# Optimization experiments

Hardware: AMD Instinct MI355X
Metric: run time of the kernel (lower is better)

Reference implementation:

```python
import jax, jax.numpy as jnp
import numpy as np

B, S, HID = 2, 2048, 1024
H, HKV, D = 16, 8, 128
G = H // HKV
EPS = 1e-6
ROPE_BASE = 1e6


def _rms_norm(x, w):
    # per-last-dim RMSNorm in fp32, matching QwenRMSNorm
    x32 = x.astype(jnp.float32)
    var = jnp.mean(x32 * x32, axis=-1, keepdims=True)
    return w * (x32 * jax.lax.rsqrt(var + EPS)).astype(x.dtype)


def _rotate_half(x):
    half = x.shape[-1] // 2
    return jnp.concatenate([-x[..., half:], x[..., :half]], axis=-1)


def setup_inputs() -> dict:
    key = jax.random.key(0)
    ks = jax.random.split(key, 6)
    return {
        "hidden_states": jax.random.normal(ks[0], (B, S, HID), dtype=jnp.float32),
        "position_ids": jnp.arange(S, dtype=jnp.int32),
        "Wq": jax.random.normal(ks[1], (HID, H * D), dtype=jnp.float32) * 0.02,
        "Wk": jax.random.normal(ks[2], (HID, HKV * D), dtype=jnp.float32) * 0.02,
        "Wv": jax.random.normal(ks[3], (HID, HKV * D), dtype=jnp.float32) * 0.02,
        "Wo": jax.random.normal(ks[4], (H * D, HID), dtype=jnp.float32) * 0.02,
        "q_norm_w": jnp.ones((D,), dtype=jnp.float32),
        "k_norm_w": jnp.ones((D,), dtype=jnp.float32),
    }


def reference(hidden_states, position_ids, Wq, Wk, Wv, Wo, q_norm_w, k_norm_w):
    b, s, _ = hidden_states.shape
    # projections
    q = (hidden_states @ Wq).reshape(b, s, H, D)
    k = (hidden_states @ Wk).reshape(b, s, HKV, D)
    v = (hidden_states @ Wv).reshape(b, s, HKV, D)
    # QK RMSNorm (per head_dim), then [B, heads, S, D]
    q = _rms_norm(q, q_norm_w).transpose(0, 2, 1, 3)
    k = _rms_norm(k, k_norm_w).transpose(0, 2, 1, 3)
    v = v.transpose(0, 2, 1, 3)
    # RoPE
    inv_freq = 1.0 / (ROPE_BASE ** (jnp.arange(0, D, 2, dtype=jnp.float32) / D))
    freqs = position_ids.astype(jnp.float32)[:, None] * inv_freq[None, :]  # [S, D/2]
    emb = jnp.concatenate([freqs, freqs], axis=-1)  # [S, D]
    cos = jnp.cos(emb)[None, None, :, :].astype(q.dtype)
    sin = jnp.sin(emb)[None, None, :, :].astype(q.dtype)
    q = q * cos + _rotate_half(q) * sin
    k = k * cos + _rotate_half(k) * sin
    # GQA attention without materializing repeated K/V:
    # q heads h = kh*G + g  <->  repeat_interleave(G, dim=1) of kv heads
    qg = q.reshape(b, HKV, G, s, D)
    scale = 1.0 / jnp.sqrt(jnp.asarray(D, dtype=q.dtype))
    scores = jnp.einsum('bhgqd,bhkd->bhgqk', qg, k) * scale  # [B,HKV,G,S,S]
    causal = jnp.tril(jnp.ones((s, s), dtype=bool))
    scores = jnp.where(causal[None, None, None, :, :], scores, jnp.finfo(scores.dtype).min)
    probs = jax.nn.softmax(scores, axis=-1)
    attn = jnp.einsum('bhgqk,bhkd->bhgqd', probs, v)  # [B,HKV,G,S,D]
    attn = attn.reshape(b, H, s, D).transpose(0, 2, 1, 3).reshape(b, s, H * D)
    out = attn @ Wo
    return out, k, v
```

## Files before the change

### kernel.cpp

```cpp
#include <hip/hip_runtime.h>

#define B_ 2
#define S_ 2048
#define HID_ 1024
#define H_ 16
#define HKV_ 8
#define D_ 128

typedef unsigned short u16;
typedef __attribute__((ext_vector_type(8))) short short8;
typedef __attribute__((ext_vector_type(4))) float f32x4;
typedef __attribute__((ext_vector_type(16))) float f32x16;
typedef __attribute__((ext_vector_type(2))) unsigned short u16x2;
typedef __attribute__((ext_vector_type(4))) unsigned short u16x4;
typedef const __attribute__((address_space(1))) void gvoid;
typedef __attribute__((address_space(3))) void svoid;

__device__ __forceinline__ u16 f2b(float f) {
  union { float f; unsigned u; } v; v.f = f;
  unsigned r = v.u + 0x7FFFu + ((v.u >> 16) & 1u);
  return (u16)(r >> 16);
}
__device__ __forceinline__ float b2f(u16 x) {
  union { unsigned u; float f; } v; v.u = ((unsigned)x) << 16; return v.f;
}

__device__ __forceinline__ float exp2_fast(float x) {
  float r; asm("v_exp_f32 %0, %1" : "=v"(r) : "v"(x)); return r;
}
__device__ __forceinline__ unsigned cvtpk_bf16(float lo, float hi) {
  unsigned r; asm("v_cvt_pk_bf16_f32 %0, %1, %2" : "=v"(r) : "v"(lo), "v"(hi)); return r;
}
__device__ __forceinline__ void vm_drain() {
  asm volatile("s_waitcnt vmcnt(0)" ::: "memory");
  __builtin_amdgcn_sched_barrier(0);
}

__global__ __launch_bounds__(256) void conv_bf16_kernel(const float* __restrict__ X,
                                                        u16* __restrict__ Y, int n4) {
  int i = blockIdx.x * 256 + threadIdx.x;
  if (i < n4) {
    const float4 v = ((const float4*)X)[i];
    u16x4 o = { f2b(v.x), f2b(v.y), f2b(v.z), f2b(v.w) };
    ((u16x4*)Y)[i] = o;
  }
}

template <bool PERM>
__global__ __launch_bounds__(256) void transpose_bf16_kernel(const float* __restrict__ W,
                                                             u16* __restrict__ Wt,
                                                             int K, int N) {
  __shared__ float t[32][33];
  const int nb = N >> 5;
  const int bx = blockIdx.x % nb;
  const int by = blockIdx.x / nb;
  const int tx = threadIdx.x & 31, ty = threadIdx.x >> 5;
#pragma unroll
  for (int i = 0; i < 32; i += 8)
    t[ty + i][tx] = W[(size_t)(by * 32 + ty + i) * N + bx * 32 + tx];
  __syncthreads();
#pragma unroll
  for (int i = 0; i < 32; i += 8) {
    int n = bx * 32 + ty + i;
    int nn;
    if (PERM) {
      int head = n >> 7, d = n & 127;
      int p = (d & 15) | (((d >> 6) & 1) << 4) | (((d >> 4) & 1) << 5) | (((d >> 5) & 1) << 6);
      nn = head * 128 + p;
    } else {
      nn = n;
    }
    Wt[(size_t)nn * K + by * 32 + tx] = f2b(t[tx][ty + i]);
  }
}

__global__ __launch_bounds__(256) void rope_table_kernel(const int* __restrict__ pid,
                                                         float* __restrict__ ct,
                                                         float* __restrict__ st) {
  int i = blockIdx.x * 256 + threadIdx.x;
  if (i >= 64 * S_) return;
  int f = i >> 11, s = i & 2047;
  double inv = exp2(-(double)f * (19.931568569324174 / 64.0));
  double ang = (double)pid[s] * inv;
  ct[i] = (float)cos(ang);
  st[i] = (float)sin(ang);
}

template <int M, int N, int K, int BM>
__global__ __launch_bounds__(256) void gemm_bt(const u16* __restrict__ A,
                                               const u16* __restrict__ Bt,
                                               float* __restrict__ C) {
  __shared__ u16 As[BM * 32];
  __shared__ u16 Bs[128 * 32];
  const int tid = threadIdx.x;
  const int w = tid >> 6;
  const int l = tid & 63;
  const int l15 = l & 15, lg = l >> 4;
  const int nbx = N / 128;
  const int bx = blockIdx.x % nbx, by = blockIdx.x / nbx;
  const int row0 = by * BM, col0 = bx * 128;
  const int wr = w >> 1, wc = w & 1;
  constexpr int MR = BM / 32;

  f32x4 acc[MR][4];
#pragma unroll
  for (int m = 0; m < MR; ++m)
#pragma unroll
    for (int n = 0; n < 4; ++n) acc[m][n] = (f32x4){0.f, 0.f, 0.f, 0.f};

  for (int k0 = 0; k0 < K; k0 += 32) {
    __syncthreads();
#pragma unroll
    for (int i = 0; i < BM / 64; ++i) {
      int c = i * 256 + tid;
      int r = c >> 2, cc = c & 3;
      const u16* sa = A + (size_t)(row0 + r) * K + k0 + cc * 8;
      __builtin_amdgcn_global_load_lds((gvoid*)sa, (svoid*)(As + (i * 256 + w * 64) * 8), 16, 0, 0);
    }
#pragma unroll
    for (int i = 0; i < 2; ++i) {
      int c = i * 256 + tid;
      int r = c >> 2, cc = c & 3;
      const u16* sb = Bt + (size_t)(col0 + r) * K + k0 + cc * 8;
      __builtin_amdgcn_global_load_lds((gvoid*)sb, (svoid*)(Bs + (i * 256 + w * 64) * 8), 16, 0, 0);
    }
    vm_drain();
    __syncthreads();
    short8 af[MR], bf[4];
#pragma unroll
    for (int m = 0; m < MR; ++m)
      af[m] = *(const short8*)(As + (wr * (BM / 2) + m * 16 + l15) * 32 + lg * 8);
#pragma unroll
    for (int n = 0; n < 4; ++n)
      bf[n] = *(const short8*)(Bs + (wc * 64 + n * 16 + l15) * 32 + lg * 8);
#pragma unroll
    for (int m = 0; m < MR; ++m)
#pragma unroll
      for (int n = 0; n < 4; ++n)
        acc[m][n] = __builtin_amdgcn_mfma_f32_16x16x32_bf16(af[m], bf[n], acc[m][n], 0, 0, 0);
  }
#pragma unroll
  for (int m = 0; m < MR; ++m)
#pragma unroll
    for (int n = 0; n < 4; ++n) {
      float* cp = C + (size_t)(row0 + wr * (BM / 2) + m * 16 + lg * 4) * N + col0 + wc * 64 + n * 16 + l15;
#pragma unroll
      for (int r = 0; r < 4; ++r) cp[(size_t)r * N] = acc[m][n][r];
    }
}

__global__ __launch_bounds__(256) void gemm_qkv_fused(const u16* __restrict__ A,
                                                      const u16* __restrict__ Bt,
                                                      const float* __restrict__ qnw,
                                                      const float* __restrict__ knw,
                                                      const float* __restrict__ ct_t,
                                                      const float* __restrict__ st_t,
                                                      u16* __restrict__ Qbb,
                                                      u16* __restrict__ Kbb,
                                                      float* __restrict__ kout,
                                                      float* __restrict__ vout,
                                                      u16* __restrict__ VTb) {
  constexpr int K = 1024;
  __shared__ u16 As[128 * 32];
  __shared__ u16 Bs[128 * 32];
  __shared__ float red[128][2];
  const int tid = threadIdx.x;
  const int w = tid >> 6;
  const int l = tid & 63;
  const int l15 = l & 15, lg = l >> 4;
  const int bx = blockIdx.x & 31, by = blockIdx.x >> 5;
  const int row0 = by * 128, col0 = bx * 128;
  const int wr = w >> 1, wc = w & 1;

  f32x4 acc[4][4];
#pragma unroll
  for (int m = 0; m < 4; ++m)
#pragma unroll
    for (int n = 0; n < 4; ++n) acc[m][n] = (f32x4){0.f, 0.f, 0.f, 0.f};

  for (int k0 = 0; k0 < K; k0 += 32) {
    __syncthreads();
#pragma unroll
    for (int i = 0; i < 2; ++i) {
      int c = i * 256 + tid;
      int r = c >> 2, cc = c & 3;
      const u16* sa = A + (size_t)(row0 + r) * K + k0 + cc * 8;
      __builtin_amdgcn_global_load_lds((gvoid*)sa, (svoid*)(As + (i * 256 + w * 64) * 8), 16, 0, 0);
      const u16* sb = Bt + (size_t)(col0 + r) * K + k0 + cc * 8;
      __builtin_amdgcn_global_load_lds((gvoid*)sb, (svoid*)(Bs + (i * 256 + w * 64) * 8), 16, 0, 0);
    }
    vm_drain();
    __syncthreads();
    short8 af[4], bf[4];
#pragma unroll
    for (int m = 0; m < 4; ++m)
      af[m] = *(const short8*)(As + (wr * 64 + m * 16 + l15) * 32 + lg * 8);
#pragma unroll
    for (int n = 0; n < 4; ++n)
      bf[n] = *(const short8*)(Bs + (wc * 64 + n * 16 + l15) * 32 + lg * 8);
#pragma unroll
    for (int m = 0; m < 4; ++m)
#pragma unroll
      for (int n = 0; n < 4; ++n)
        acc[m][n] = __builtin_amdgcn_mfma_f32_16x16x32_bf16(af[m], bf[n], acc[m][n], 0, 0, 0);
  }

  const int b_ = row0 >> 11;
  const int s0 = row0 & 2047;
  if (bx < 24) {
    float part[4][4];
#pragma unroll
    for (int m = 0; m < 4; ++m)
#pragma unroll
      for (int r = 0; r < 4; ++r) {
        float p = 0.f;
#pragma unroll
        for (int n = 0; n < 4; ++n) p += acc[m][n][r] * acc[m][n][r];
        part[m][r] = p;
      }
#pragma unroll
    for (int i = 1; i < 16; i <<= 1)
#pragma unroll
      for (int m = 0; m < 4; ++m)
#pragma unroll
        for (int r = 0; r < 4; ++r) part[m][r] += __shfl_xor(part[m][r], i, 64);
    if (l15 == 0) {
#pragma unroll
      for (int m = 0; m < 4; ++m)
#pragma unroll
        for (int r = 0; r < 4; ++r) red[wr * 64 + m * 16 + lg * 4 + r][wc] = part[m][r];
    }
    __syncthreads();

    const bool isQ = bx < 16;
    const int h = isQ ? bx : bx - 16;
    const float* nw = isQ ? qnw : knw;
    u16* outb = isQ ? Qbb : Kbb;
    const int NH = isQ ? 16 : 8;
#pragma unroll
    for (int np = 0; np < 2; ++np) {
      const int d_lo = l15 + 32 * wc + 16 * np;
      const float w_lo = nw[d_lo], w_hi = nw[d_lo + 64];
#pragma unroll
      for (int m = 0; m < 4; ++m) {
        const int sb = s0 + wr * 64 + m * 16 + lg * 4;
        const float4 cv = *(const float4*)(ct_t + d_lo * 2048 + sb);
        const float4 sv = *(const float4*)(st_t + d_lo * 2048 + sb);
#pragma unroll
        for (int r = 0; r < 4; ++r) {
          const int ro = wr * 64 + m * 16 + lg * 4 + r;
          const float tot = red[ro][0] + red[ro][1];
          const float rms = rsqrtf(tot * (1.0f / 128.0f) + 1e-6f);
          const float xl = acc[m][2 * np][r] * rms * w_lo;
          const float xh = acc[m][2 * np + 1][r] * rms * w_hi;
          const float cc = ((const float*)&cv)[r], ss = ((const float*)&sv)[r];
          const float ol = xl * cc - xh * ss;
          const float oh = xh * cc + xl * ss;
          const size_t base = ((size_t)(b_ * NH + h) * 2048 + sb + r) * 128;
          outb[base + d_lo] = f2b(ol);
          outb[base + d_lo + 64] = f2b(oh);
          if (!isQ) {
            kout[base + d_lo] = ol;
            kout[base + d_lo + 64] = oh;
          }
        }
      }
    }
  } else {
    const int h = bx - 24;
#pragma unroll
    for (int n = 0; n < 4; ++n) {
      const int d = wc * 64 + n * 16 + l15;
#pragma unroll
      for (int m = 0; m < 4; ++m) {
        const int sb = s0 + wr * 64 + m * 16 + lg * 4;
        u16x4 pk;
#pragma unroll
        for (int r = 0; r < 4; ++r) {
          const float x = acc[m][n][r];
          vout[((size_t)(b_ * 8 + h) * 2048 + sb + r) * 128 + d] = x;
          pk[r] = f2b(x);
        }
        *(u16x4*)(VTb + ((size_t)(b_ * 8 + h) * 128 + d) * 2048 + sb) = pk;
      }
    }
  }
}

__global__ __launch_bounds__(256, 2) void attn_kernel(const u16* __restrict__ Qb,
                                                      const u16* __restrict__ Kb,
                                                      const u16* __restrict__ VTb,
                                                      u16* __restrict__ Ab,
                                                      u16* __restrict__ Op,
                                                      float* __restrict__ Ml) {
  __shared__ u16 lds[2][16384];
  const int tid = threadIdx.x;
  const int w = tid >> 6, l = tid & 63;
  const int l31 = l & 31, hi = l >> 5;
  const int bid = blockIdx.x;
  const int half = bid & 1;
  const int pid = bid >> 1;
  const int b = pid >> 7;
  const int hh = (pid >> 3) & 15;
  const int p8 = pid & 7;
  const int hkv = hh >> 1;

  const u16* Kh = Kb + (size_t)(b * HKV_ + hkv) * S_ * 128;
  const u16* VTh = VTb + (size_t)(b * HKV_ + hkv) * 128 * S_;
  const float KSC = 0.12751740027f;
  int cur = 0;

  auto stage = [&](int kt, int buf) {
    const u16* Kp = Kh + (size_t)kt * 64 * 128;
    const u16* Vp = VTh + kt * 64;
    u16* Kd = &lds[buf][0];
    u16* Vd = &lds[buf][8192];
#pragma unroll
    for (int i = 0; i < 4; ++i) {
      int c = i * 256 + tid;
      int kr = c >> 4, kc = c & 15;
      int kcs = kc ^ ((kr ^ (kr >> 3)) & 15);
      __builtin_amdgcn_global_load_lds((gvoid*)(Kp + kr * 128 + kcs * 8),
                                       (svoid*)(Kd + (i * 256 + w * 64) * 8), 16, 0, 0);
      int vd = c >> 3, vc = c & 7;
      int vcs = vc ^ ((vd ^ (vd >> 3)) & 7);
      __builtin_amdgcn_global_load_lds((gvoid*)(Vp + (size_t)vd * S_ + vcs * 8),
                                       (svoid*)(Vd + (i * 256 + w * 64) * 8), 16, 0, 0);
    }
  };

  auto run_seg = [&](int pp, int kt0, int kt1, int mode) {
    const int q0 = pp * 128;
    const int ntp = 2 * (pp + 1);
    const int qrow = q0 + w * 32 + l31;

    short8 qf[8];
    {
      const u16* qp = Qb + ((size_t)(b * H_ + hh) * S_ + qrow) * 128 + hi * 8;
#pragma unroll
      for (int c = 0; c < 8; ++c) qf[c] = *(const short8*)(qp + c * 16);
    }

    float m_run = -1e30f, l_run = 0.f;
    f32x16 oacc[4];
#pragma unroll
    for (int n = 0; n < 4; ++n)
#pragma unroll
      for (int r = 0; r < 16; ++r) oacc[n][r] = 0.f;

    stage(kt0, cur);
    vm_drain();
    __syncthreads();
    for (int kt = kt0; kt < kt1; ++kt) {
      if (kt + 1 < kt1) stage(kt + 1, cur ^ 1);
      const u16* Kl = &lds[cur][0];
      const u16* Vl = &lds[cur][8192];
      const bool domask = (kt >= ntp - 2);

#pragma unroll
      for (int ts = 0; ts < 2; ++ts) {
        f32x16 stv;
#pragma unroll
        for (int r = 0; r < 16; ++r) stv[r] = 0.f;
        {
          const int row = ts * 32 + l31;
          const int rb = row * 256, sw = ((row ^ (row >> 3)) & 15) << 4;
#pragma unroll
          for (int c = 0; c < 8; ++c) {
            short8 kf = *(const short8*)((const char*)Kl + rb + ((c * 32 + hi * 16) ^ sw));
            stv = __builtin_amdgcn_mfma_f32_32x32x16_bf16(kf, qf[c], stv, 0, 0, 0);
          }
        }

        float pvv[16];
        float mx = -1e30f;
#pragma unroll
        for (int r = 0; r < 16; ++r) {
          float x = stv[r] * KSC;
          if (domask) {
            int kv = kt * 64 + ts * 32 + (r & 3) + 8 * (r >> 2) + 4 * hi;
            if (kv > qrow) x = -1e30f;
          }
          pvv[r] = x;
          mx = fmaxf(mx, x);
        }
        mx = fmaxf(mx, __shfl_xor(mx, 32, 64));

        if (__any(mx > m_run + 8.0f)) {
          float mnew = fmaxf(m_run, mx);
          float corr = exp2_fast(m_run - mnew);
          l_run *= corr;
          m_run = mnew;
#pragma unroll
          for (int r = 0; r < 16; ++r) {
            float cr = __shfl(corr, (r & 3) + 8 * (r >> 2) + 4 * hi, 64);
#pragma unroll
            for (int n = 0; n < 4; ++n) oacc[n][r] *= cr;
          }
        }

        float ls = 0.f;
#pragma unroll
        for (int r = 0; r < 16; ++r) {
          float p = exp2_fast(pvv[r] - m_run);
          pvv[r] = p;
          ls += p;
        }
        l_run += ls + __shfl_xor(ls, 32, 64);

        unsigned W[4][2], Wx[4][2];
#pragma unroll
        for (int g = 0; g < 4; ++g)
#pragma unroll
          for (int i = 0; i < 2; ++i) {
            W[g][i] = cvtpk_bf16(pvv[4 * g + 2 * i], pvv[4 * g + 2 * i + 1]);
            Wx[g][i] = __shfl_xor(W[g][i], 32, 64);
          }

#pragma unroll
        for (int cc = 0; cc < 2; ++cc) {
          short8 paf;
          ((unsigned*)&paf)[0] = hi ? Wx[2 * cc + 1][0] : W[2 * cc][0];
          ((unsigned*)&paf)[1] = hi ? Wx[2 * cc + 1][1] : W[2 * cc][1];
          ((unsigned*)&paf)[2] = hi ? W[2 * cc + 1][0] : Wx[2 * cc][0];
          ((unsigned*)&paf)[3] = hi ? W[2 * cc + 1][1] : Wx[2 * cc][1];
          const int cp = ts * 2 + cc;
#pragma unroll
          for (int n = 0; n < 4; ++n) {
            const int d = n * 32 + l31;
            const int swv = ((d ^ (d >> 3)) & 7) << 4;
            short8 vf = *(const short8*)((const char*)Vl + d * 128 + ((cp * 32 + hi * 16) ^ swv));
            oacc[n] = __builtin_amdgcn_mfma_f32_32x32x16_bf16(paf, vf, oacc[n], 0, 0, 0);
          }
        }
      }
      vm_drain();
      __syncthreads();
      cur ^= 1;
    }

    if (mode == 0) {
#pragma unroll
      for (int r = 0; r < 16; ++r) {
        const int ql = (r & 3) + 8 * (r >> 2) + 4 * hi;
        float lb = __shfl(l_run, ql, 64);
        float inv = 1.0f / lb;
        const int q = q0 + w * 32 + ql;
        u16* op = Ab + ((size_t)(b * S_) + q) * 2048 + hh * 128 + l31;
#pragma unroll
        for (int n = 0; n < 4; ++n) op[n * 32] = f2b(oacc[n][r] * inv);
      }
    } else {
      const int part = mode - 1;
      u16* ob = Op + ((size_t)(part * 256 + pid)) * 128 * 128;
#pragma unroll
      for (int r = 0; r < 16; ++r) {
        const int ql = (r & 3) + 8 * (r >> 2) + 4 * hi;
        const int qq = w * 32 + ql;
#pragma unroll
        for (int n = 0; n < 4; ++n) ob[qq * 128 + n * 32 + l31] = f2b(oacc[n][r]);
      }
      if (hi == 0) {
        float* mlb = Ml + ((size_t)(part * 256 + pid)) * 256;
        mlb[w * 32 + l31] = m_run;
        mlb[128 + w * 32 + l31] = l_run;
      }
    }
  };

  if (half == 0) {
    run_seg(p8, 0, 2 * p8 + 2, 0);
    run_seg(15 - p8, 0, 15 - 2 * p8, 1);
  } else {
    run_seg(15 - p8, 15 - 2 * p8, 32 - 2 * p8, 2);
  }
}

__global__ __launch_bounds__(256) void attn_combine_kernel(const u16* __restrict__ Op,
                                                           const float* __restrict__ Ml,
                                                           u16* __restrict__ Ab) {
  const int pid = blockIdx.x;
  const int b = pid >> 7, hh = (pid >> 3) & 15, p8 = pid & 7;
  const int pp = 15 - p8;
  const int q = threadIdx.x >> 1;
  const int d0 = (threadIdx.x & 1) * 64;
  const float* ml0 = Ml + (size_t)pid * 256;
  const float* ml1 = Ml + (size_t)(256 + pid) * 256;
  const float m0 = ml0[q], l0 = ml0[128 + q];
  const float m1 = ml1[q], l1 = ml1[128 + q];
  const float m = fmaxf(m0, m1);
  const float w0 = exp2_fast(m0 - m), w1 = exp2_fast(m1 - m);
  const float linv = 1.0f / (w0 * l0 + w1 * l1);
  const u16* o0 = Op + ((size_t)pid * 128 + q) * 128 + d0;
  const u16* o1 = Op + ((size_t)(256 + pid) * 128 + q) * 128 + d0;
  u16* ab = Ab + ((size_t)(b * S_) + pp * 128 + q) * 2048 + hh * 128 + d0;
#pragma unroll
  for (int c = 0; c < 8; ++c) {
    short8 a = *(const short8*)(o0 + c * 8);
    short8 bb = *(const short8*)(o1 + c * 8);
    short8 o;
#pragma unroll
    for (int j = 0; j < 8; ++j)
      o[j] = (short)f2b((w0 * b2f((u16)a[j]) + w1 * b2f((u16)bb[j])) * linv);
    *(short8*)(ab + c * 8) = o;
  }
}

extern "C" void kernel_launch(void* const* d_in, const int* in_sizes, int n_in,
                              void* d_out, int out_size, void* d_ws, size_t ws_size,
                              hipStream_t stream) {
  const float* hs  = (const float*)d_in[0];
  const int*   pid = (const int*)d_in[1];
  const float* Wq  = (const float*)d_in[2];
  const float* Wk  = (const float*)d_in[3];
  const float* Wv  = (const float*)d_in[4];
  const float* Wo  = (const float*)d_in[5];
  const float* qnw = (const float*)d_in[6];
  const float* knw = (const float*)d_in[7];

  float* out0 = (float*)d_out;
  float* kout = out0 + (size_t)B_ * HKV_ * S_ * D_;
  float* vout = kout + (size_t)B_ * HKV_ * S_ * D_;

  char* ws = (char*)d_ws;
  size_t off = 0;
  auto alloc = [&](size_t bytes) {
    void* p = ws + off;
    off += (bytes + 255) & ~(size_t)255;
    return p;
  };
  u16*   Xb    = (u16*)alloc((size_t)4096 * 1024 * 2);
  u16*   Wqkvt = (u16*)alloc((size_t)4096 * 1024 * 2);
  u16*   Wot   = (u16*)alloc((size_t)1024 * 2048 * 2);
  float* ct_t  = (float*)alloc((size_t)64 * 2048 * 4);
  float* st_t  = (float*)alloc((size_t)64 * 2048 * 4);
  u16*   Qbb   = (u16*)alloc((size_t)B_ * H_ * S_ * D_ * 2);
  u16*   Kbb   = (u16*)alloc((size_t)B_ * HKV_ * S_ * D_ * 2);
  u16*   VTb   = (u16*)alloc((size_t)B_ * HKV_ * D_ * S_ * 2);
  u16*   Ab    = (u16*)alloc((size_t)B_ * S_ * H_ * D_ * 2);
  u16*   Op    = (u16*)alloc((size_t)2 * 256 * 128 * 128 * 2);
  float* Ml    = (float*)alloc((size_t)2 * 256 * 256 * 4);

  conv_bf16_kernel<<<4096, 256, 0, stream>>>(hs, Xb, 4096 * 1024 / 4);
  transpose_bf16_kernel<true><<<(2048 / 32) * (1024 / 32), 256, 0, stream>>>(Wq, Wqkvt, 1024, 2048);
  transpose_bf16_kernel<true><<<(1024 / 32) * (1024 / 32), 256, 0, stream>>>(Wk, Wqkvt + (size_t)2048 * 1024, 1024, 1024);
  transpose_bf16_kernel<false><<<(1024 / 32) * (1024 / 32), 256, 0, stream>>>(Wv, Wqkvt + (size_t)3072 * 1024, 1024, 1024);
  transpose_bf16_kernel<false><<<(1024 / 32) * (2048 / 32), 256, 0, stream>>>(Wo, Wot, 2048, 1024);
  rope_table_kernel<<<512, 256, 0, stream>>>(pid, ct_t, st_t);

  gemm_qkv_fused<<<1024, 256, 0, stream>>>(Xb, Wqkvt, qnw, knw, ct_t, st_t,
                                           Qbb, Kbb, kout, vout, VTb);

  attn_kernel<<<512, 256, 0, stream>>>(Qbb, Kbb, VTb, Ab, Op, Ml);
  attn_combine_kernel<<<256, 256, 0, stream>>>(Op, Ml, Ab);

  gemm_bt<4096, 1024, 2048, 64><<<8 * 64, 256, 0, stream>>>(Ab, Wot, out0);
}
```

Before: 182.0 us.

## Halve QKV GEMM row tile and move V transpose into separate kernel

Shrinks the fused QKV GEMM tile from 128x128 to 64x128, doubling the grid to 2048 blocks for more parallelism and lower register/LDS use per block. It also removes the strided bf16 V-transpose store from the GEMM epilogue and adds a standalone LDS-tiled transpose kernel that reads the fp32 V output and writes VTb with coalesced stores. The costs are more re-reads of the B operand across the smaller tiles, an extra kernel launch, and an extra read of V from global memory.

New measurement: 189.4 us. 4.1% more time.

```diff
diff --git a/kernel.cpp b/kernel.cpp
--- a/kernel.cpp
+++ b/kernel.cpp
@@ -158,48 +158,51 @@
                                                       u16* __restrict__ Qbb,
                                                       u16* __restrict__ Kbb,
                                                       float* __restrict__ kout,
-                                                      float* __restrict__ vout,
-                                                      u16* __restrict__ VTb) {
+                                                      float* __restrict__ vout) {
   constexpr int K = 1024;
-  __shared__ u16 As[128 * 32];
+  __shared__ u16 As[64 * 32];
   __shared__ u16 Bs[128 * 32];
-  __shared__ float red[128][2];
+  __shared__ float red[64][2];
   const int tid = threadIdx.x;
   const int w = tid >> 6;
   const int l = tid & 63;
   const int l15 = l & 15, lg = l >> 4;
   const int bx = blockIdx.x & 31, by = blockIdx.x >> 5;
-  const int row0 = by * 128, col0 = bx * 128;
+  const int row0 = by * 64, col0 = bx * 128;
   const int wr = w >> 1, wc = w & 1;
 
-  f32x4 acc[4][4];
-#pragma unroll
-  for (int m = 0; m < 4; ++m)
+  f32x4 acc[2][4];
+#pragma unroll
+  for (int m = 0; m < 2; ++m)
 #pragma unroll
     for (int n = 0; n < 4; ++n) acc[m][n] = (f32x4){0.f, 0.f, 0.f, 0.f};
 
   for (int k0 = 0; k0 < K; k0 += 32) {
     __syncthreads();
+    {
+      int c = tid;
+      int r = c >> 2, cc = c & 3;
+      const u16* sa = A + (size_t)(row0 + r) * K + k0 + cc * 8;
+      __builtin_amdgcn_global_load_lds((gvoid*)sa, (svoid*)(As + (w * 64) * 8), 16, 0, 0);
+    }
 #pragma unroll
     for (int i = 0; i < 2; ++i) {
       int c = i * 256 + tid;
       int r = c >> 2, cc = c & 3;
-      const u16* sa = A + (size_t)(row0 + r) * K + k0 + cc * 8;
-      __builtin_amdgcn_global_load_lds((gvoid*)sa, (svoid*)(As + (i * 256 + w * 64) * 8), 16, 0, 0);
       const u16* sb = Bt + (size_t)(col0 + r) * K + k0 + cc * 8;
       __builtin_amdgcn_global_load_lds((gvoid*)sb, (svoid*)(Bs + (i * 256 + w * 64) * 8), 16, 0, 0);
     }
     vm_drain();
     __syncthreads();
-    short8 af[4], bf[4];
-#pragma unroll
-    for (int m = 0; m < 4; ++m)
-      af[m] = *(const short8*)(As + (wr * 64 + m * 16 + l15) * 32 + lg * 8);
+    short8 af[2], bf[4];
+#pragma unroll
+    for (int m = 0; m < 2; ++m)
+      af[m] = *(const short8*)(As + (wr * 32 + m * 16 + l15) * 32 + lg * 8);
 #pragma unroll
     for (int n = 0; n < 4; ++n)
       bf[n] = *(const short8*)(Bs + (wc * 64 + n * 16 + l15) * 32 + lg * 8);
 #pragma unroll
-    for (int m = 0; m < 4; ++m)
+    for (int m = 0; m < 2; ++m)
 #pragma unroll
       for (int n = 0; n < 4; ++n)
         acc[m][n] = __builtin_amdgcn_mfma_f32_16x16x32_bf16(af[m], bf[n], acc[m][n], 0, 0, 0);
@@ -208,9 +211,9 @@
   const int b_ = row0 >> 11;
   const int s0 = row0 & 2047;
   if (bx < 24) {
-    float part[4][4];
-#pragma unroll
-    for (int m = 0; m < 4; ++m)
+    float part[2][4];
+#pragma unroll
+    for (int m = 0; m < 2; ++m)
 #pragma unroll
       for (int r = 0; r < 4; ++r) {
         float p = 0.f;
@@ -221,14 +224,14 @@
 #pragma unroll
     for (int i = 1; i < 16; i <<= 1)
 #pragma unroll
-      for (int m = 0; m < 4; ++m)
+      for (int m = 0; m < 2; ++m)
 #pragma unroll
         for (int r = 0; r < 4; ++r) part[m][r] += __shfl_xor(part[m][r], i, 64);
     if (l15 == 0) {
 #pragma unroll
-      for (int m = 0; m < 4; ++m)
-#pragma unroll
-        for (int r = 0; r < 4; ++r) red[wr * 64 + m * 16 + lg * 4 + r][wc] = part[m][r];
+      for (int m = 0; m < 2; ++m)
+#pragma unroll
+        for (int r = 0; r < 4; ++r) red[wr * 32 + m * 16 + lg * 4 + r][wc] = part[m][r];
     }
     __syncthreads();
 
@@ -242,13 +245,13 @@
       const int d_lo = l15 + 32 * wc + 16 * np;
       const float w_lo = nw[d_lo], w_hi = nw[d_lo + 64];
 #pragma unroll
-      for (int m = 0; m < 4; ++m) {
-        const int sb = s0 + wr * 64 + m * 16 + lg * 4;
+      for (int m = 0; m < 2; ++m) {
+        const int sb = s0 + wr * 32 + m * 16 + lg * 4;
         const float4 cv = *(const float4*)(ct_t + d_lo * 2048 + sb);
         const float4 sv = *(const float4*)(st_t + d_lo * 2048 + sb);
 #pragma unroll
         for (int r = 0; r < 4; ++r) {
-          const int ro = wr * 64 + m * 16 + lg * 4 + r;
+          const int ro = wr * 32 + m * 16 + lg * 4 + r;
           const float tot = red[ro][0] + red[ro][1];
           const float rms = rsqrtf(tot * (1.0f / 128.0f) + 1e-6f);
           const float xl = acc[m][2 * np][r] * rms * w_lo;
@@ -272,18 +275,34 @@
     for (int n = 0; n < 4; ++n) {
       const int d = wc * 64 + n * 16 + l15;
 #pragma unroll
-      for (int m = 0; m < 4; ++m) {
-        const int sb = s0 + wr * 64 + m * 16 + lg * 4;
-        u16x4 pk;
-#pragma unroll
-        for (int r = 0; r < 4; ++r) {
-          const float x = acc[m][n][r];
-          vout[((size_t)(b_ * 8 + h) * 2048 + sb + r) * 128 + d] = x;
-          pk[r] = f2b(x);
-        }
-        *(u16x4*)(VTb + ((size_t)(b_ * 8 + h) * 128 + d) * 2048 + sb) = pk;
-      }
-    }
+      for (int m = 0; m < 2; ++m) {
+        const int sb = s0 + wr * 32 + m * 16 + lg * 4;
+#pragma unroll
+        for (int r = 0; r < 4; ++r)
+          vout[((size_t)(b_ * 8 + h) * 2048 + sb + r) * 128 + d] = acc[m][n][r];
+      }
+    }
+  }
+}
+
+__global__ __launch_bounds__(256) void vtrans2_kernel(const float* __restrict__ vout,
+                                                      u16* __restrict__ VTb) {
+  __shared__ float t[32][33];
+  const int bid = blockIdx.x;
+  const int stile = bid & 63;
+  const int dt = (bid >> 6) & 3;
+  const int bh = bid >> 8;
+  const int tx = threadIdx.x & 31, ty = threadIdx.x >> 5;
+#pragma unroll
+  for (int j = 0; j < 4; ++j) {
+    int s = stile * 32 + ty + 8 * j;
+    t[ty + 8 * j][tx] = vout[((size_t)bh * 2048 + s) * 128 + dt * 32 + tx];
+  }
+  __syncthreads();
+#pragma unroll
+  for (int j = 0; j < 4; ++j) {
+    int d = dt * 32 + ty + 8 * j;
+    VTb[((size_t)bh * 128 + d) * 2048 + stile * 32 + tx] = f2b(t[tx][ty + 8 * j]);
   }
 }
 
@@ -548,8 +567,9 @@
   transpose_bf16_kernel<false><<<(1024 / 32) * (2048 / 32), 256, 0, stream>>>(Wo, Wot, 2048, 1024);
   rope_table_kernel<<<512, 256, 0, stream>>>(pid, ct_t, st_t);
 
-  gemm_qkv_fused<<<1024, 256, 0, stream>>>(Xb, Wqkvt, qnw, knw, ct_t, st_t,
-                                           Qbb, Kbb, kout, vout, VTb);
+  gemm_qkv_fused<<<2048, 256, 0, stream>>>(Xb, Wqkvt, qnw, knw, ct_t, st_t,
+                                           Qbb, Kbb, kout, vout);
+  vtrans2_kernel<<<4096, 256, 0, stream>>>(vout, VTb);
 
   attn_kernel<<<512, 256, 0, stream>>>(Qbb, Kbb, VTb, Ab, Op, Ml);
   attn_combine_kernel<<<256, 256, 0, stream>>>(Op, Ml, Ab);
```
